# Performance work log

Hardware: AMD Instinct MI355X
Metric: run time of the kernel (lower is better)

Reference implementation:

```python
import jax, jax.numpy as jnp
import numpy as np

N_FEATURES = 64
EMB = 32
HID = 2 * EMB  # 64
B, T = 256, 2048


def _lstm(x, W_ih, W_hh, b_ih, b_hh):
    """PyTorch-convention single-layer LSTM. x: [B,T,F]. Gate order: i,f,g,o.
    Returns (outputs [B,T,H], final_hidden [B,H])."""
    H = W_hh.shape[1]
    # Precompute input projections for all timesteps in one big GEMM.
    pre = jnp.einsum('btf,gf->btg', x, W_ih) + b_ih + b_hh  # [B,T,4H]
    h0 = jnp.zeros((x.shape[0], H), dtype=x.dtype)
    c0 = jnp.zeros((x.shape[0], H), dtype=x.dtype)

    def step(carry, p):
        h, c = carry
        gates = p + h @ W_hh.T  # [B,4H]
        i, f, g, o = jnp.split(gates, 4, axis=-1)
        i = jax.nn.sigmoid(i)
        f = jax.nn.sigmoid(f)
        g = jnp.tanh(g)
        o = jax.nn.sigmoid(o)
        c = f * c + i * g
        h = o * jnp.tanh(c)
        return (h, c), h

    (hT, _), hs = jax.lax.scan(step, (h0, c0), pre.transpose(1, 0, 2))
    return hs.transpose(1, 0, 2), hT


def _forward_one(x, W_ih1, W_hh1, b_ih1, b_hh1, W_ih2, W_hh2, b_ih2, b_hh2):
    y, _ = _lstm(x, W_ih1, W_hh1, b_ih1, b_hh1)
    _, hT = _lstm(y, W_ih2, W_hh2, b_ih2, b_hh2)
    return hT  # [B, EMB] == hidden_n.reshape(B, n_layers*embedding_dim)


def setup_inputs() -> dict:
    key = jax.random.key(0)
    ks = jax.random.split(key, 10)
    s = 0.1
    return {
        'x1': jax.random.normal(ks[0], (B, T, N_FEATURES), dtype=jnp.float32),
        'x2': jax.random.normal(ks[1], (B, T, N_FEATURES), dtype=jnp.float32),
        'W_ih1': jax.random.normal(ks[2], (4 * HID, N_FEATURES), dtype=jnp.float32) * s,
        'W_hh1': jax.random.normal(ks[3], (4 * HID, HID), dtype=jnp.float32) * s,
        'b_ih1': jax.random.normal(ks[4], (4 * HID,), dtype=jnp.float32) * s,
        'b_hh1': jax.random.normal(ks[5], (4 * HID,), dtype=jnp.float32) * s,
        'W_ih2': jax.random.normal(ks[6], (4 * EMB, HID), dtype=jnp.float32) * s,
        'W_hh2': jax.random.normal(ks[7], (4 * EMB, EMB), dtype=jnp.float32) * s,
        'b_ih2': jax.random.normal(ks[8], (4 * EMB,), dtype=jnp.float32) * s,
        'b_hh2': jax.random.normal(ks[9], (4 * EMB,), dtype=jnp.float32) * s,
    }


def reference(x1, x2, W_ih1, W_hh1, b_ih1, b_hh1, W_ih2, W_hh2, b_ih2, b_hh2):
    emb1 = _forward_one(x1, W_ih1, W_hh1, b_ih1, b_hh1, W_ih2, W_hh2, b_ih2, b_hh2)
    emb2 = _forward_one(x2, W_ih1, W_hh1, b_ih1, b_hh1, W_ih2, W_hh2, b_ih2, b_hh2)
    return (emb1, emb2)
```

## Files before the change

### kernel.cpp

```cpp
#include <hip/hip_runtime.h>

#define TT 2048

typedef _Float16 f16;
typedef _Float16 f16x2 __attribute__((ext_vector_type(2)));
typedef unsigned int u32;

static __device__ __forceinline__ float fdot2f(u32 a, u32 b, float c) {
  return __builtin_amdgcn_fdot2(__builtin_bit_cast(f16x2, a),
                                __builtin_bit_cast(f16x2, b), c, false);
}
static __device__ __forceinline__ u32 packh2(float a, float b) {
  f16x2 v; v[0] = (f16)a; v[1] = (f16)b;
  return __builtin_bit_cast(u32, v);
}
static __device__ __forceinline__ float sigm(float x) {
  return 1.f / (1.f + __expf(-x));
}
static __device__ __forceinline__ float tanh_(float x) {
  x = fminf(15.f, fmaxf(-15.f, x));
  const float e = __expf(2.f * x);
  return (e - 1.f) / (e + 1.f);
}

__launch_bounds__(192, 2)
__global__ void lstm2_pc_kernel(const float* __restrict__ x1,
                                const float* __restrict__ x2,
                                const float* __restrict__ Wih1,
                                const float* __restrict__ Whh1,
                                const float* __restrict__ bih1,
                                const float* __restrict__ bhh1,
                                const float* __restrict__ Wih2,
                                const float* __restrict__ Whh2,
                                const float* __restrict__ bih2,
                                const float* __restrict__ bhh2,
                                float* __restrict__ out)
{
  __shared__ u32 s_x[32];
  __shared__ u32 s_h1[2][32];
  __shared__ u32 s_h2[16];
  __shared__ float s_pre[4][256];

  const int tid = threadIdx.x;
  const int lane = tid & 63;
  const int wid = tid >> 6;
  const int bid = blockIdx.x;
  const int which = bid >> 8;
  const int row = bid & 255;
  const float* __restrict__ xg = (which ? x2 : x1) + row * (TT * 64) + lane;

  u32 w[4][32];
  float bias[4] = {0.f, 0.f, 0.f, 0.f};

  if (wid == 0) {
    #pragma unroll
    for (int g = 0; g < 4; ++g) {
      const float* src = Wih1 + (lane + 64 * g) * 64;
      #pragma unroll
      for (int kp = 0; kp < 32; ++kp) {
        const float2 v = *(const float2*)(src + 2 * kp);
        w[g][kp] = packh2(v.x, v.y);
      }
      bias[g] = bih1[lane + 64 * g] + bhh1[lane + 64 * g];
    }
  } else if (wid == 1) {
    #pragma unroll
    for (int g = 0; g < 4; ++g) {
      const float* src = Whh1 + (lane + 64 * g) * 64;
      #pragma unroll
      for (int kp = 0; kp < 32; ++kp) {
        const float2 v = *(const float2*)(src + 2 * kp);
        w[g][kp] = packh2(v.x, v.y);
      }
    }
    if (lane < 32) s_h1[1][lane] = 0u;
  } else {
    #pragma unroll
    for (int g = 0; g < 2; ++g) {
      const float* src = Wih2 + (lane + 64 * g) * 64;
      #pragma unroll
      for (int kp = 0; kp < 32; ++kp) {
        const float2 v = *(const float2*)(src + 2 * kp);
        w[g][kp] = packh2(v.x, v.y);
      }
      const float* s2 = Whh2 + (lane + 64 * g) * 32;
      #pragma unroll
      for (int kp = 0; kp < 16; ++kp) {
        const float2 v = *(const float2*)(s2 + 2 * kp);
        w[2 + g][kp] = packh2(v.x, v.y);
      }
      #pragma unroll
      for (int kp = 16; kp < 32; ++kp) w[2 + g][kp] = 0u;
      bias[g] = bih2[lane + 64 * g] + bhh2[lane + 64 * g];
    }
    if (lane < 16) s_h2[lane] = 0u;
  }

  float c1 = 0.f, c2 = 0.f;
  float xA = 0.f, xB = 0.f;

  if (wid == 0) {
    #pragma unroll
    for (int p = 0; p < 2; ++p) {
      ((f16*)s_x)[lane] = (f16)xg[p * 64];
      float a0 = bias[0], a1 = bias[1], a2 = bias[2], a3 = bias[3];
      #pragma unroll
      for (int q = 0; q < 8; ++q) {
        const uint4 xv = *(const uint4*)&s_x[4 * q];
        a0 = fdot2f(w[0][4*q+0], xv.x, a0); a1 = fdot2f(w[1][4*q+0], xv.x, a1);
        a2 = fdot2f(w[2][4*q+0], xv.x, a2); a3 = fdot2f(w[3][4*q+0], xv.x, a3);
        a0 = fdot2f(w[0][4*q+1], xv.y, a0); a1 = fdot2f(w[1][4*q+1], xv.y, a1);
        a2 = fdot2f(w[2][4*q+1], xv.y, a2); a3 = fdot2f(w[3][4*q+1], xv.y, a3);
        a0 = fdot2f(w[0][4*q+2], xv.z, a0); a1 = fdot2f(w[1][4*q+2], xv.z, a1);
        a2 = fdot2f(w[2][4*q+2], xv.z, a2); a3 = fdot2f(w[3][4*q+2], xv.z, a3);
        a0 = fdot2f(w[0][4*q+3], xv.w, a0); a1 = fdot2f(w[1][4*q+3], xv.w, a1);
        a2 = fdot2f(w[2][4*q+3], xv.w, a2); a3 = fdot2f(w[3][4*q+3], xv.w, a3);
      }
      s_pre[p][lane]       = a0;
      s_pre[p][lane + 64]  = a1;
      s_pre[p][lane + 128] = a2;
      s_pre[p][lane + 192] = a3;
    }
    xA = xg[2 * 64];
    xB = xg[3 * 64];
  }
  __syncthreads();

  #pragma unroll 1
  for (int i = 0; i <= TT; ++i) {
    if (wid == 0) {
      if (i + 2 < TT) {
        ((f16*)s_x)[lane] = (f16)xA;
        xA = xB;
        xB = (i + 4 < TT) ? xg[(i + 4) * 64] : 0.f;
        float a0 = bias[0], a1 = bias[1], a2 = bias[2], a3 = bias[3];
        #pragma unroll
        for (int q = 0; q < 8; ++q) {
          const uint4 xv = *(const uint4*)&s_x[4 * q];
          a0 = fdot2f(w[0][4*q+0], xv.x, a0); a1 = fdot2f(w[1][4*q+0], xv.x, a1);
          a2 = fdot2f(w[2][4*q+0], xv.x, a2); a3 = fdot2f(w[3][4*q+0], xv.x, a3);
          a0 = fdot2f(w[0][4*q+1], xv.y, a0); a1 = fdot2f(w[1][4*q+1], xv.y, a1);
          a2 = fdot2f(w[2][4*q+1], xv.y, a2); a3 = fdot2f(w[3][4*q+1], xv.y, a3);
          a0 = fdot2f(w[0][4*q+2], xv.z, a0); a1 = fdot2f(w[1][4*q+2], xv.z, a1);
          a2 = fdot2f(w[2][4*q+2], xv.z, a2); a3 = fdot2f(w[3][4*q+2], xv.z, a3);
          a0 = fdot2f(w[0][4*q+3], xv.w, a0); a1 = fdot2f(w[1][4*q+3], xv.w, a1);
          a2 = fdot2f(w[2][4*q+3], xv.w, a2); a3 = fdot2f(w[3][4*q+3], xv.w, a3);
        }
        const int sl = (i + 2) & 3;
        s_pre[sl][lane]       = a0;
        s_pre[sl][lane + 64]  = a1;
        s_pre[sl][lane + 128] = a2;
        s_pre[sl][lane + 192] = a3;
      }
    } else if (wid == 1) {
      if (i < TT) {
        const float* pr = s_pre[i & 3];
        float a0 = pr[lane], a1 = pr[lane + 64];
        float a2 = pr[lane + 128], a3 = pr[lane + 192];
        const u32* hp = s_h1[(i + 1) & 1];
        #pragma unroll
        for (int q = 0; q < 8; ++q) {
          const uint4 hv = *(const uint4*)&hp[4 * q];
          a0 = fdot2f(w[0][4*q+0], hv.x, a0); a1 = fdot2f(w[1][4*q+0], hv.x, a1);
          a2 = fdot2f(w[2][4*q+0], hv.x, a2); a3 = fdot2f(w[3][4*q+0], hv.x, a3);
          a0 = fdot2f(w[0][4*q+1], hv.y, a0); a1 = fdot2f(w[1][4*q+1], hv.y, a1);
          a2 = fdot2f(w[2][4*q+1], hv.y, a2); a3 = fdot2f(w[3][4*q+1], hv.y, a3);
          a0 = fdot2f(w[0][4*q+2], hv.z, a0); a1 = fdot2f(w[1][4*q+2], hv.z, a1);
          a2 = fdot2f(w[2][4*q+2], hv.z, a2); a3 = fdot2f(w[3][4*q+2], hv.z, a3);
          a0 = fdot2f(w[0][4*q+3], hv.w, a0); a1 = fdot2f(w[1][4*q+3], hv.w, a1);
          a2 = fdot2f(w[2][4*q+3], hv.w, a2); a3 = fdot2f(w[3][4*q+3], hv.w, a3);
        }
        const float i1 = sigm(a0), f1 = sigm(a1), g1 = tanh_(a2), o1 = sigm(a3);
        c1 = f1 * c1 + i1 * g1;
        const float h1v = o1 * tanh_(c1);
        ((f16*)s_h1[i & 1])[lane] = (f16)h1v;
      }
    } else {
      if (i > 0) {
        const int t = i - 1;
        float b0 = bias[0], b1_ = bias[1];
        const u32* hp = s_h1[t & 1];
        #pragma unroll
        for (int q = 0; q < 8; ++q) {
          const uint4 hv = *(const uint4*)&hp[4 * q];
          b0 = fdot2f(w[0][4*q+0], hv.x, b0); b1_ = fdot2f(w[1][4*q+0], hv.x, b1_);
          b0 = fdot2f(w[0][4*q+1], hv.y, b0); b1_ = fdot2f(w[1][4*q+1], hv.y, b1_);
          b0 = fdot2f(w[0][4*q+2], hv.z, b0); b1_ = fdot2f(w[1][4*q+2], hv.z, b1_);
          b0 = fdot2f(w[0][4*q+3], hv.w, b0); b1_ = fdot2f(w[1][4*q+3], hv.w, b1_);
        }
        #pragma unroll
        for (int q = 0; q < 4; ++q) {
          const uint4 hv = *(const uint4*)&s_h2[4 * q];
          b0 = fdot2f(w[2][4*q+0], hv.x, b0); b1_ = fdot2f(w[3][4*q+0], hv.x, b1_);
          b0 = fdot2f(w[2][4*q+1], hv.y, b0); b1_ = fdot2f(w[3][4*q+1], hv.y, b1_);
          b0 = fdot2f(w[2][4*q+2], hv.z, b0); b1_ = fdot2f(w[3][4*q+2], hv.z, b1_);
          b0 = fdot2f(w[2][4*q+3], hv.w, b0); b1_ = fdot2f(w[3][4*q+3], hv.w, b1_);
        }
        const float p0 = __shfl_xor(b0, 32, 64);
        const float p1 = __shfl_xor(b1_, 32, 64);
        const bool lo = lane < 32;
        const float gi = lo ? b0  : p0;
        const float gf = lo ? p0  : b0;
        const float gg = lo ? b1_ : p1;
        const float go = lo ? p1  : b1_;
        const float i2 = sigm(gi), f2 = sigm(gf), g2v = tanh_(gg), o2 = sigm(go);
        c2 = f2 * c2 + i2 * g2v;
        const float h2v = o2 * tanh_(c2);
        if (lo) ((f16*)s_h2)[lane] = (f16)h2v;
        if (t == TT - 1 && lo) out[which * 8192 + row * 32 + lane] = h2v;
      }
    }
    __syncthreads();
  }
}

extern "C" void kernel_launch(void* const* d_in, const int* in_sizes, int n_in,
                              void* d_out, int out_size, void* d_ws, size_t ws_size,
                              hipStream_t stream) {
  const float* x1   = (const float*)d_in[0];
  const float* x2   = (const float*)d_in[1];
  const float* Wih1 = (const float*)d_in[2];
  const float* Whh1 = (const float*)d_in[3];
  const float* bih1 = (const float*)d_in[4];
  const float* bhh1 = (const float*)d_in[5];
  const float* Wih2 = (const float*)d_in[6];
  const float* Whh2 = (const float*)d_in[7];
  const float* bih2 = (const float*)d_in[8];
  const float* bhh2 = (const float*)d_in[9];
  float* out = (float*)d_out;

  lstm2_pc_kernel<<<dim3(512), dim3(192), 0, stream>>>(
      x1, x2, Wih1, Whh1, bih1, bhh1, Wih2, Whh2, bih2, bhh2, out);
}
```

Baseline: 1.787 ms.

## Rewrite LSTM kernel with MFMA batching 16 sequences per block

Replaces the per-sequence fdot2 kernel (512 blocks of 192 threads) with an MFMA-based kernel where each block handles 16 batch rows. Four waves compute layer-1 gates with 16x16x32 f16 MFMAs, two waves compute layer 2, and a seventh wave streams x through an 8-slot LDS ring with register prefetch. This turns per-step dot products into matrix ops and amortizes weights across rows. The grid shrinks to only 32 blocks, so most of the device sits idle and the serial per-step latency of each block decides the runtime.

```diff
diff --git a/kernel.cpp b/kernel.cpp
--- a/kernel.cpp
+++ b/kernel.cpp
@@ -4,15 +4,19 @@
 
 typedef _Float16 f16;
 typedef _Float16 f16x2 __attribute__((ext_vector_type(2)));
+typedef _Float16 f16x8 __attribute__((ext_vector_type(8)));
+typedef float f32x4 __attribute__((ext_vector_type(4)));
 typedef unsigned int u32;
 
-static __device__ __forceinline__ float fdot2f(u32 a, u32 b, float c) {
-  return __builtin_amdgcn_fdot2(__builtin_bit_cast(f16x2, a),
-                                __builtin_bit_cast(f16x2, b), c, false);
-}
 static __device__ __forceinline__ u32 packh2(float a, float b) {
   f16x2 v; v[0] = (f16)a; v[1] = (f16)b;
   return __builtin_bit_cast(u32, v);
+}
+static __device__ __forceinline__ uint4 pack8(float4 a, float4 b) {
+  uint4 r;
+  r.x = packh2(a.x, a.y); r.y = packh2(a.z, a.w);
+  r.z = packh2(b.x, b.y); r.w = packh2(b.z, b.w);
+  return r;
 }
 static __device__ __forceinline__ float sigm(float x) {
   return 1.f / (1.f + __expf(-x));
@@ -22,195 +26,194 @@
   const float e = __expf(2.f * x);
   return (e - 1.f) / (e + 1.f);
 }
-
-__launch_bounds__(192, 2)
-__global__ void lstm2_pc_kernel(const float* __restrict__ x1,
-                                const float* __restrict__ x2,
-                                const float* __restrict__ Wih1,
-                                const float* __restrict__ Whh1,
-                                const float* __restrict__ bih1,
-                                const float* __restrict__ bhh1,
-                                const float* __restrict__ Wih2,
-                                const float* __restrict__ Whh2,
-                                const float* __restrict__ bih2,
-                                const float* __restrict__ bhh2,
-                                float* __restrict__ out)
+static __device__ __forceinline__ f16x8 ldwfrag(const float* __restrict__ W,
+                                                int row, int ld, int kbase) {
+  const float* p = W + row * ld + kbase;
+  const float4 a = *(const float4*)p;
+  const float4 b = *(const float4*)(p + 4);
+  f16x8 r;
+  r[0]=(f16)a.x; r[1]=(f16)a.y; r[2]=(f16)a.z; r[3]=(f16)a.w;
+  r[4]=(f16)b.x; r[5]=(f16)b.y; r[6]=(f16)b.z; r[7]=(f16)b.w;
+  return r;
+}
+static __device__ __forceinline__ f32x4 MF(f16x8 a, f16x8 b, f32x4 c) {
+  return __builtin_amdgcn_mfma_f32_16x16x32_f16(a, b, c, 0, 0, 0);
+}
+
+__launch_bounds__(448, 1)
+__global__ void lstm2_mfma_kernel(const float* __restrict__ x1,
+                                  const float* __restrict__ x2,
+                                  const float* __restrict__ Wih1,
+                                  const float* __restrict__ Whh1,
+                                  const float* __restrict__ bih1,
+                                  const float* __restrict__ bhh1,
+                                  const float* __restrict__ Wih2,
+                                  const float* __restrict__ Whh2,
+                                  const float* __restrict__ bih2,
+                                  const float* __restrict__ bhh2,
+                                  float* __restrict__ out)
 {
-  __shared__ u32 s_x[32];
-  __shared__ u32 s_h1[2][32];
-  __shared__ u32 s_h2[16];
-  __shared__ float s_pre[4][256];
+  __shared__ __align__(16) u32 s_ring[8][512];
+  __shared__ __align__(16) f16 s_h1[2][16][72];
+  __shared__ __align__(16) f16 s_h2[2][16][40];
 
   const int tid = threadIdx.x;
-  const int lane = tid & 63;
+  const int l = tid & 63;
   const int wid = tid >> 6;
+  const int ln = l & 15;
+  const int lg = l >> 4;
   const int bid = blockIdx.x;
-  const int which = bid >> 8;
-  const int row = bid & 255;
-  const float* __restrict__ xg = (which ? x2 : x1) + row * (TT * 64) + lane;
-
-  u32 w[4][32];
-  float bias[4] = {0.f, 0.f, 0.f, 0.f};
-
-  if (wid == 0) {
-    #pragma unroll
-    for (int g = 0; g < 4; ++g) {
-      const float* src = Wih1 + (lane + 64 * g) * 64;
+  const int which = bid >> 4;
+  const int rowbase = (bid & 15) * 16;
+
+  for (int idx = tid; idx < 16 * 72; idx += 448) ((f16*)s_h1[1])[idx] = (f16)0.f;
+  for (int idx = tid; idx < 16 * 40; idx += 448) ((f16*)s_h2[1])[idx] = (f16)0.f;
+
+  f16x8 wx[4][2];
+  f16x8 wh[4][2];
+  float bs[4] = {0.f, 0.f, 0.f, 0.f};
+  #pragma unroll
+  for (int q = 0; q < 4; ++q) { wx[q][0] = wx[q][1] = wh[q][0] = wh[q][1] = (f16x8)(f16)0.f; }
+
+  if (wid < 4) {
+    #pragma unroll
+    for (int q = 0; q < 4; ++q) {
+      const int g = 64 * q + 16 * wid + ln;
       #pragma unroll
-      for (int kp = 0; kp < 32; ++kp) {
-        const float2 v = *(const float2*)(src + 2 * kp);
-        w[g][kp] = packh2(v.x, v.y);
+      for (int c = 0; c < 2; ++c) {
+        wx[q][c] = ldwfrag(Wih1, g, 64, 32 * c + lg * 8);
+        wh[q][c] = ldwfrag(Whh1, g, 64, 32 * c + lg * 8);
       }
-      bias[g] = bih1[lane + 64 * g] + bhh1[lane + 64 * g];
-    }
-  } else if (wid == 1) {
-    #pragma unroll
-    for (int g = 0; g < 4; ++g) {
-      const float* src = Whh1 + (lane + 64 * g) * 64;
+      bs[q] = bih1[g] + bhh1[g];
+    }
+  } else if (wid < 6) {
+    const int w2 = wid - 4;
+    #pragma unroll
+    for (int q = 0; q < 4; ++q) {
+      const int g = 32 * q + 16 * w2 + ln;
       #pragma unroll
-      for (int kp = 0; kp < 32; ++kp) {
-        const float2 v = *(const float2*)(src + 2 * kp);
-        w[g][kp] = packh2(v.x, v.y);
-      }
-    }
-    if (lane < 32) s_h1[1][lane] = 0u;
-  } else {
-    #pragma unroll
-    for (int g = 0; g < 2; ++g) {
-      const float* src = Wih2 + (lane + 64 * g) * 64;
-      #pragma unroll
-      for (int kp = 0; kp < 32; ++kp) {
-        const float2 v = *(const float2*)(src + 2 * kp);
-        w[g][kp] = packh2(v.x, v.y);
-      }
-      const float* s2 = Whh2 + (lane + 64 * g) * 32;
-      #pragma unroll
-      for (int kp = 0; kp < 16; ++kp) {
-        const float2 v = *(const float2*)(s2 + 2 * kp);
-        w[2 + g][kp] = packh2(v.x, v.y);
-      }
-      #pragma unroll
-      for (int kp = 16; kp < 32; ++kp) w[2 + g][kp] = 0u;
-      bias[g] = bih2[lane + 64 * g] + bhh2[lane + 64 * g];
-    }
-    if (lane < 16) s_h2[lane] = 0u;
+      for (int c = 0; c < 2; ++c) wx[q][c] = ldwfrag(Wih2, g, 64, 32 * c + lg * 8);
+      wh[q][0] = ldwfrag(Whh2, g, 32, lg * 8);
+      bs[q] = bih2[g] + bhh2[g];
+    }
   }
 
-  float c1 = 0.f, c2 = 0.f;
-  float xA = 0.f, xB = 0.f;
-
-  if (wid == 0) {
+  const int uu = 16 * ((wid < 4) ? wid : (wid - 4)) + ln;
+  float cc[4] = {0.f, 0.f, 0.f, 0.f};
+
+  float4 xb[4][4];
+  uint4 u4[4][2];
+  const float* __restrict__ xrow =
+      (which ? x2 : x1) + (size_t)(rowbase + ln) * (TT * 64);
+  if (wid == 6) {
     #pragma unroll
     for (int p = 0; p < 2; ++p) {
-      ((f16*)s_x)[lane] = (f16)xg[p * 64];
-      float a0 = bias[0], a1 = bias[1], a2 = bias[2], a3 = bias[3];
-      #pragma unroll
-      for (int q = 0; q < 8; ++q) {
-        const uint4 xv = *(const uint4*)&s_x[4 * q];
-        a0 = fdot2f(w[0][4*q+0], xv.x, a0); a1 = fdot2f(w[1][4*q+0], xv.x, a1);
-        a2 = fdot2f(w[2][4*q+0], xv.x, a2); a3 = fdot2f(w[3][4*q+0], xv.x, a3);
-        a0 = fdot2f(w[0][4*q+1], xv.y, a0); a1 = fdot2f(w[1][4*q+1], xv.y, a1);
-        a2 = fdot2f(w[2][4*q+1], xv.y, a2); a3 = fdot2f(w[3][4*q+1], xv.y, a3);
-        a0 = fdot2f(w[0][4*q+2], xv.z, a0); a1 = fdot2f(w[1][4*q+2], xv.z, a1);
-        a2 = fdot2f(w[2][4*q+2], xv.z, a2); a3 = fdot2f(w[3][4*q+2], xv.z, a3);
-        a0 = fdot2f(w[0][4*q+3], xv.w, a0); a1 = fdot2f(w[1][4*q+3], xv.w, a1);
-        a2 = fdot2f(w[2][4*q+3], xv.w, a2); a3 = fdot2f(w[3][4*q+3], xv.w, a3);
-      }
-      s_pre[p][lane]       = a0;
-      s_pre[p][lane + 64]  = a1;
-      s_pre[p][lane + 128] = a2;
-      s_pre[p][lane + 192] = a3;
-    }
-    xA = xg[2 * 64];
-    xB = xg[3 * 64];
+      const float* ps = xrow + p * 64;
+      const float4 a0 = *(const float4*)(ps + lg * 8);
+      const float4 a1 = *(const float4*)(ps + lg * 8 + 4);
+      const float4 b0 = *(const float4*)(ps + 32 + lg * 8);
+      const float4 b1 = *(const float4*)(ps + 32 + lg * 8 + 4);
+      *(uint4*)&s_ring[p][lg * 64 + ln * 4] = pack8(a0, a1);
+      *(uint4*)&s_ring[p][256 + lg * 64 + ln * 4] = pack8(b0, b1);
+    }
+    #pragma unroll
+    for (int b = 0; b < 4; ++b) {
+      const float* ps = xrow + (2 + b) * 64;
+      xb[b][0] = *(const float4*)(ps + lg * 8);
+      xb[b][1] = *(const float4*)(ps + lg * 8 + 4);
+      xb[b][2] = *(const float4*)(ps + 32 + lg * 8);
+      xb[b][3] = *(const float4*)(ps + 32 + lg * 8 + 4);
+    }
   }
   __syncthreads();
 
   #pragma unroll 1
-  for (int i = 0; i <= TT; ++i) {
-    if (wid == 0) {
-      if (i + 2 < TT) {
-        ((f16*)s_x)[lane] = (f16)xA;
-        xA = xB;
-        xB = (i + 4 < TT) ? xg[(i + 4) * 64] : 0.f;
-        float a0 = bias[0], a1 = bias[1], a2 = bias[2], a3 = bias[3];
-        #pragma unroll
-        for (int q = 0; q < 8; ++q) {
-          const uint4 xv = *(const uint4*)&s_x[4 * q];
-          a0 = fdot2f(w[0][4*q+0], xv.x, a0); a1 = fdot2f(w[1][4*q+0], xv.x, a1);
-          a2 = fdot2f(w[2][4*q+0], xv.x, a2); a3 = fdot2f(w[3][4*q+0], xv.x, a3);
-          a0 = fdot2f(w[0][4*q+1], xv.y, a0); a1 = fdot2f(w[1][4*q+1], xv.y, a1);
-          a2 = fdot2f(w[2][4*q+1], xv.y, a2); a3 = fdot2f(w[3][4*q+1], xv.y, a3);
-          a0 = fdot2f(w[0][4*q+2], xv.z, a0); a1 = fdot2f(w[1][4*q+2], xv.z, a1);
-          a2 = fdot2f(w[2][4*q+2], xv.z, a2); a3 = fdot2f(w[3][4*q+2], xv.z, a3);
-          a0 = fdot2f(w[0][4*q+3], xv.w, a0); a1 = fdot2f(w[1][4*q+3], xv.w, a1);
-          a2 = fdot2f(w[2][4*q+3], xv.w, a2); a3 = fdot2f(w[3][4*q+3], xv.w, a3);
-        }
-        const int sl = (i + 2) & 3;
-        s_pre[sl][lane]       = a0;
-        s_pre[sl][lane + 64]  = a1;
-        s_pre[sl][lane + 128] = a2;
-        s_pre[sl][lane + 192] = a3;
+  for (int ii = 0; ii <= TT; ii += 4) {
+    #pragma unroll
+    for (int r = 0; r < 4; ++r) {
+      const int i = ii + r;
+      if (wid < 4) {
+        if (i < TT) {
+          const u32* rs = s_ring[i & 7];
+          const f16x8 xa0 = *(const f16x8*)&rs[lg * 64 + ln * 4];
+          const f16x8 xa1 = *(const f16x8*)&rs[256 + lg * 64 + ln * 4];
+          const f16* hb = &s_h1[(i + 1) & 1][ln][lg * 8];
+          const f16x8 ha0 = *(const f16x8*)hb;
+          const f16x8 ha1 = *(const f16x8*)(hb + 32);
+          f32x4 a0 = {bs[0], bs[0], bs[0], bs[0]};
+          f32x4 a1 = {bs[1], bs[1], bs[1], bs[1]};
+          f32x4 a2 = {bs[2], bs[2], bs[2], bs[2]};
+          f32x4 a3 = {bs[3], bs[3], bs[3], bs[3]};
+          a0 = MF(xa0, wx[0][0], a0); a1 = MF(xa0, wx[1][0], a1);
+          a2 = MF(xa0, wx[2][0], a2); a3 = MF(xa0, wx[3][0], a3);
+          a0 = MF(xa1, wx[0][1], a0); a1 = MF(xa1, wx[1][1], a1);
+          a2 = MF(xa1, wx[2][1], a2); a3 = MF(xa1, wx[3][1], a3);
+          a0 = MF(ha0, wh[0][0], a0); a1 = MF(ha0, wh[1][0], a1);
+          a2 = MF(ha0, wh[2][0], a2); a3 = MF(ha0, wh[3][0], a3);
+          a0 = MF(ha1, wh[0][1], a0); a1 = MF(ha1, wh[1][1], a1);
+          a2 = MF(ha1, wh[2][1], a2); a3 = MF(ha1, wh[3][1], a3);
+          #pragma unroll
+          for (int r2 = 0; r2 < 4; ++r2) {
+            const float gi = sigm(a0[r2]), gf = sigm(a1[r2]);
+            const float gg = tanh_(a2[r2]), go = sigm(a3[r2]);
+            cc[r2] = gf * cc[r2] + gi * gg;
+            const float hv = go * tanh_(cc[r2]);
+            s_h1[i & 1][lg * 4 + r2][uu] = (f16)hv;
+          }
+        }
+      } else if (wid < 6) {
+        if (i >= 1 && i <= TT) {
+          const int t = i - 1;
+          const f16* hb = &s_h1[t & 1][ln][lg * 8];
+          const f16x8 ha0 = *(const f16x8*)hb;
+          const f16x8 ha1 = *(const f16x8*)(hb + 32);
+          const f16x8 g0 = *(const f16x8*)&s_h2[(t + 1) & 1][ln][lg * 8];
+          f32x4 b0 = {bs[0], bs[0], bs[0], bs[0]};
+          f32x4 b1 = {bs[1], bs[1], bs[1], bs[1]};
+          f32x4 b2 = {bs[2], bs[2], bs[2], bs[2]};
+          f32x4 b3 = {bs[3], bs[3], bs[3], bs[3]};
+          b0 = MF(ha0, wx[0][0], b0); b1 = MF(ha0, wx[1][0], b1);
+          b2 = MF(ha0, wx[2][0], b2); b3 = MF(ha0, wx[3][0], b3);
+          b0 = MF(ha1, wx[0][1], b0); b1 = MF(ha1, wx[1][1], b1);
+          b2 = MF(ha1, wx[2][1], b2); b3 = MF(ha1, wx[3][1], b3);
+          b0 = MF(g0, wh[0][0], b0);  b1 = MF(g0, wh[1][0], b1);
+          b2 = MF(g0, wh[2][0], b2);  b3 = MF(g0, wh[3][0], b3);
+          #pragma unroll
+          for (int r2 = 0; r2 < 4; ++r2) {
+            const float gi = sigm(b0[r2]), gf = sigm(b1[r2]);
+            const float gg = tanh_(b2[r2]), go = sigm(b3[r2]);
+            cc[r2] = gf * cc[r2] + gi * gg;
+            const float hv = go * tanh_(cc[r2]);
+            s_h2[t & 1][lg * 4 + r2][uu] = (f16)hv;
+            if (t == TT - 1)
+              out[which * 8192 + (rowbase + lg * 4 + r2) * 32 + uu] = hv;
+          }
+        }
+      } else {
+        if (r == 0) {
+          #pragma unroll
+          for (int b = 0; b < 4; ++b) {
+            u4[b][0] = pack8(xb[b][0], xb[b][1]);
+            u4[b][1] = pack8(xb[b][2], xb[b][3]);
+          }
+          #pragma unroll
+          for (int b = 0; b < 4; ++b) {
+            int s = ii + 6 + b; if (s > TT - 1) s = TT - 1;
+            const float* ps = xrow + s * 64;
+            xb[b][0] = *(const float4*)(ps + lg * 8);
+            xb[b][1] = *(const float4*)(ps + lg * 8 + 4);
+            xb[b][2] = *(const float4*)(ps + 32 + lg * 8);
+            xb[b][3] = *(const float4*)(ps + 32 + lg * 8 + 4);
+          }
+        }
+        if (i + 2 < TT) {
+          u32* rd = s_ring[(i + 2) & 7];
+          *(uint4*)&rd[lg * 64 + ln * 4] = u4[r][0];
+          *(uint4*)&rd[256 + lg * 64 + ln * 4] = u4[r][1];
+        }
       }
-    } else if (wid == 1) {
-      if (i < TT) {
-        const float* pr = s_pre[i & 3];
-        float a0 = pr[lane], a1 = pr[lane + 64];
-        float a2 = pr[lane + 128], a3 = pr[lane + 192];
-        const u32* hp = s_h1[(i + 1) & 1];
-        #pragma unroll
-        for (int q = 0; q < 8; ++q) {
-          const uint4 hv = *(const uint4*)&hp[4 * q];
-          a0 = fdot2f(w[0][4*q+0], hv.x, a0); a1 = fdot2f(w[1][4*q+0], hv.x, a1);
-          a2 = fdot2f(w[2][4*q+0], hv.x, a2); a3 = fdot2f(w[3][4*q+0], hv.x, a3);
-          a0 = fdot2f(w[0][4*q+1], hv.y, a0); a1 = fdot2f(w[1][4*q+1], hv.y, a1);
-          a2 = fdot2f(w[2][4*q+1], hv.y, a2); a3 = fdot2f(w[3][4*q+1], hv.y, a3);
-          a0 = fdot2f(w[0][4*q+2], hv.z, a0); a1 = fdot2f(w[1][4*q+2], hv.z, a1);
-          a2 = fdot2f(w[2][4*q+2], hv.z, a2); a3 = fdot2f(w[3][4*q+2], hv.z, a3);
-          a0 = fdot2f(w[0][4*q+3], hv.w, a0); a1 = fdot2f(w[1][4*q+3], hv.w, a1);
-          a2 = fdot2f(w[2][4*q+3], hv.w, a2); a3 = fdot2f(w[3][4*q+3], hv.w, a3);
-        }
-        const float i1 = sigm(a0), f1 = sigm(a1), g1 = tanh_(a2), o1 = sigm(a3);
-        c1 = f1 * c1 + i1 * g1;
-        const float h1v = o1 * tanh_(c1);
-        ((f16*)s_h1[i & 1])[lane] = (f16)h1v;
-      }
-    } else {
-      if (i > 0) {
-        const int t = i - 1;
-        float b0 = bias[0], b1_ = bias[1];
-        const u32* hp = s_h1[t & 1];
-        #pragma unroll
-        for (int q = 0; q < 8; ++q) {
-          const uint4 hv = *(const uint4*)&hp[4 * q];
-          b0 = fdot2f(w[0][4*q+0], hv.x, b0); b1_ = fdot2f(w[1][4*q+0], hv.x, b1_);
-          b0 = fdot2f(w[0][4*q+1], hv.y, b0); b1_ = fdot2f(w[1][4*q+1], hv.y, b1_);
-          b0 = fdot2f(w[0][4*q+2], hv.z, b0); b1_ = fdot2f(w[1][4*q+2], hv.z, b1_);
-          b0 = fdot2f(w[0][4*q+3], hv.w, b0); b1_ = fdot2f(w[1][4*q+3], hv.w, b1_);
-        }
-        #pragma unroll
-        for (int q = 0; q < 4; ++q) {
-          const uint4 hv = *(const uint4*)&s_h2[4 * q];
-          b0 = fdot2f(w[2][4*q+0], hv.x, b0); b1_ = fdot2f(w[3][4*q+0], hv.x, b1_);
-          b0 = fdot2f(w[2][4*q+1], hv.y, b0); b1_ = fdot2f(w[3][4*q+1], hv.y, b1_);
-          b0 = fdot2f(w[2][4*q+2], hv.z, b0); b1_ = fdot2f(w[3][4*q+2], hv.z, b1_);
-          b0 = fdot2f(w[2][4*q+3], hv.w, b0); b1_ = fdot2f(w[3][4*q+3], hv.w, b1_);
-        }
-        const float p0 = __shfl_xor(b0, 32, 64);
-        const float p1 = __shfl_xor(b1_, 32, 64);
-        const bool lo = lane < 32;
-        const float gi = lo ? b0  : p0;
-        const float gf = lo ? p0  : b0;
-        const float gg = lo ? b1_ : p1;
-        const float go = lo ? p1  : b1_;
-        const float i2 = sigm(gi), f2 = sigm(gf), g2v = tanh_(gg), o2 = sigm(go);
-        c2 = f2 * c2 + i2 * g2v;
-        const float h2v = o2 * tanh_(c2);
-        if (lo) ((f16*)s_h2)[lane] = (f16)h2v;
-        if (t == TT - 1 && lo) out[which * 8192 + row * 32 + lane] = h2v;
-      }
-    }
-    __syncthreads();
+      __syncthreads();
+    }
   }
 }
 
@@ -229,6 +232,6 @@
   const float* bhh2 = (const float*)d_in[9];
   float* out = (float*)d_out;
 
-  lstm2_pc_kernel<<<dim3(512), dim3(192), 0, stream>>>(
+  lstm2_mfma_kernel<<<dim3(32), dim3(448), 0, stream>>>(
       x1, x2, Wih1, Whh1, bih1, bhh1, Wih2, Whh2, bih2, bhh2, out);
 }
```

Measured after the change: 3.106 ms. 73.8% more time.
